# Performance work log

Measured on AMD Instinct MI355X. Metric: run time of the kernel, lower is better.

Reference implementation:

```python
import jax, jax.numpy as jnp
import numpy as np

# physical / numerical constants (from __init__ kwargs)
RHO, G, FD = 910.0, 9.81, 3.1e-17      # ice density, gravity, SIA fluidity (Pa^-3 yr^-1 units folded in)
DX = DY = 100.0                          # grid spacing [m]
DTMAX, CFL = 0.1, 0.2                    # max timestep [yr], CFL safety factor
T0, TIME0, TTOT = 1864.0, 1979.0, 1981.0 # calendar origin, start time, end time
T_FREQ = 10.0                            # SMB refresh interval [yr]
GAMMA, Z_REF = 6.0e-3, 1500.0            # temperature lapse rate [K/m], station elevation [m]
N_STEPS = 64                             # fixed unrolled step budget (while-loop -> masked scan)
NY = NX = 512
N_YEARS, N_DAYS = 128, 365


def setup_inputs() -> dict:
    key = jax.random.key(0)
    k = jax.random.split(key, 6)
    y = jnp.linspace(-1.0, 1.0, NY)
    x = jnp.linspace(-1.0, 1.0, NX)
    X, Y = jnp.meshgrid(x, y)
    r2 = X ** 2 + Y ** 2
    Z_topo = 1500.0 + 1800.0 * jnp.exp(-3.0 * r2) + 20.0 * jax.random.normal(k[0], (NY, NX))
    H_init = 50.0 * jnp.exp(-6.0 * r2)
    ice_mask = (Z_topo > 1800.0).astype(jnp.float32)
    d = jnp.arange(N_DAYS, dtype=jnp.float32)
    season = -2.0 + 12.0 * jnp.sin(2.0 * jnp.pi * (d - 120.0) / 365.0)
    T_daily = season[None, :] + 1.5 * jax.random.normal(k[1], (N_YEARS, N_DAYS))
    P_daily = 0.02 * jax.random.uniform(k[2], (N_YEARS, N_DAYS))
    precip_tensor = jax.random.uniform(k[3], (NY, NX))
    return dict(Z_topo=Z_topo.astype(jnp.float32), H_init=H_init.astype(jnp.float32),
                ice_mask=ice_mask, precip_tensor=precip_tensor,
                T_m_lowest=jnp.array([-2.0], jnp.float32), T_s=jnp.array([12.0], jnp.float32),
                P_daily=P_daily.astype(jnp.float32), T_daily=T_daily.astype(jnp.float32),
                melt_factor=jnp.array([0.005], jnp.float32))


def _smb(Z_surf, P_day, T_day, mf, ice_mask):
    """Degree-day SMB: lapse-rate downscale station daily T/P to the grid. [365,ny,nx] broadcast."""
    T = T_day[:, None, None] - GAMMA * (Z_surf - Z_REF)[None, :, :]
    acc = jnp.sum(jnp.where(T <= 0.0, P_day[:, None, None], 0.0), axis=0)   # snow accumulation [m/yr]
    pdd = jnp.sum(jnp.maximum(T, 0.0), axis=0)                               # positive degree days
    smb = (acc - mf * pdd) * ice_mask
    return jnp.where((smb < 0.0) | (ice_mask > 0.5), smb, -10.0)


def _sia_step(H, Z_topo, smb, t):
    """One adaptive-dt shallow-ice (n=3) explicit stencil step."""
    S = Z_topo + H
    gy, gx = jnp.gradient(S, DY, DX)
    D = FD * (RHO * G) ** 3 * H ** 5 * (gx ** 2 + gy ** 2)   # diffusivity at cell centers
    Dx = 0.5 * (D[:, 1:] + D[:, :-1]); Sx = (S[:, 1:] - S[:, :-1]) / DX
    Dy = 0.5 * (D[1:, :] + D[:-1, :]); Sy = (S[1:, :] - S[:-1, :]) / DY
    qx = jnp.pad(Dx * Sx, ((0, 0), (1, 1)))                   # zero-flux boundaries
    qy = jnp.pad(Dy * Sy, ((1, 1), (0, 0)))
    div = (qx[:, 1:] - qx[:, :-1]) / DX + (qy[1:, :] - qy[:-1, :]) / DY
    dt = jnp.minimum(DTMAX, CFL * min(DX, DY) ** 2 / (jnp.max(D) + 1e-6))   # adaptive timestep
    H_new = jnp.maximum(H + dt * (smb + div), 0.0)
    return H_new, Z_topo + H_new, t + dt


def reference(Z_topo, H_init, ice_mask, precip_tensor, T_m_lowest, T_s, P_daily, T_daily, melt_factor):
    mf = jnp.squeeze(melt_factor)
    n_years = P_daily.shape[0]

    def year_idx(t):
        return jnp.clip(jnp.floor(t - T0), 0, n_years - 1).astype(jnp.int32)

    time0 = jnp.array(TIME0, jnp.float32)
    yi0 = year_idx(time0)
    smb0 = _smb(Z_topo + H_init, P_daily[yi0], T_daily[yi0], mf, ice_mask)
    zeros = jnp.zeros_like(H_init)
    carry0 = (H_init, Z_topo + H_init, time0, smb0, yi0, jnp.array(0.0, jnp.float32),
              zeros, zeros, zeros, jnp.array(False), jnp.array(False), jnp.array(False))

    def body(carry, _):
        H, Zs, t, smb, prev_yi, t_last, s26, s57, s80, g26, g57, g80 = carry
        active = t < TTOT
        Hn, Zsn, tn = _sia_step(H, Z_topo, smb, t)
        Hn = jnp.where(active, Hn, H)
        Zsn = jnp.where(active, Zsn, Zs)
        tn = jnp.where(active, tn, t)

        def snap(s, g, yr):
            hit = active & (tn >= yr)
            return jnp.where(hit & (~g), Hn, s), g | hit
        s26, g26 = snap(s26, g26, 1926.0)
        s57, g57 = snap(s57, g57, 1957.0)
        s80, g80 = snap(s80, g80, 1980.0)

        yi = year_idx(tn)
        need = active & ((yi != prev_yi) | (tn - t_last >= T_FREQ))
        smb_n = jax.lax.cond(need,
                             lambda: _smb(Zsn, P_daily[yi], T_daily[yi], mf, ice_mask),
                             lambda: smb)
        t_last_n = jnp.where(need, tn, t_last)
        prev_yi_n = jnp.where(need, yi, prev_yi)
        return (Hn, Zsn, tn, smb_n, prev_yi_n, t_last_n, s26, s57, s80, g26, g57, g80), None

    carry, _ = jax.lax.scan(jax.checkpoint(body), carry0, None, length=N_STEPS)
    H, _, _, _, _, _, s26, s57, s80, _, _, _ = carry
    return (s26, s57, s80, H)
```

## Files before the change

kernel.cpp:

```cpp
#include <hip/hip_runtime.h>
#include <hip/hip_bf16.h>

namespace {
constexpr int NYg = 512, NXg = 512, NCELL = NYg * NXg;
constexpr int TPB = 1024;
constexpr int NBX = 16, NBY = 16, NBLK = 256;
constexpr int BT = 32;
constexpr int W  = 10;
constexpr int NT = BT + 2 * W;
constexpr int NU = NT - 4;
constexpr int NT2 = NT * NT, NU2 = NU * NU;
constexpr int ITT = 3;
constexpr int NGH = 1476;
constexpr int KG = 5;
constexpr int NSTEP = 64;
constexpr int NEX = 32;
constexpr int DYNLDS = 34816;
constexpr float I1HX = 0.01f;
constexpr float I2HX = 0.005f;
constexpr double RGd = 910.0 * 9.81;
constexpr float PHYS_C = (float)(3.1e-17 * RGd * RGd * RGd);
}

__device__ float    g_H[2][NCELL];
__device__ unsigned g_sflag[NEX][NBLK];
__device__ unsigned g_bmax[NSTEP][NBLK];
__device__ unsigned g_barC = 0, g_barG = 0;

__device__ __forceinline__ void gen_barrier() {
    __syncthreads();
    if (threadIdx.x == 0) {
        __threadfence();
        const unsigned gen = __hip_atomic_load(&g_barG, __ATOMIC_RELAXED,
                                               __HIP_MEMORY_SCOPE_AGENT);
        const unsigned arrived = __hip_atomic_fetch_add(&g_barC, 1u, __ATOMIC_ACQ_REL,
                                                        __HIP_MEMORY_SCOPE_AGENT);
        if (arrived == NBLK - 1) {
            __hip_atomic_store(&g_barC, 0u, __ATOMIC_RELAXED, __HIP_MEMORY_SCOPE_AGENT);
            __hip_atomic_fetch_add(&g_barG, 1u, __ATOMIC_RELEASE, __HIP_MEMORY_SCOPE_AGENT);
        } else {
            while (__hip_atomic_load(&g_barG, __ATOMIC_ACQUIRE,
                                     __HIP_MEMORY_SCOPE_AGENT) == gen)
                __builtin_amdgcn_s_sleep(2);
        }
        __threadfence();
    }
    __syncthreads();
}

__device__ __forceinline__ void coh_store(float* p, float v) {
    __hip_atomic_store(p, v, __ATOMIC_RELAXED, __HIP_MEMORY_SCOPE_AGENT);
}
__device__ __forceinline__ float coh_load(const float* p) {
    return __hip_atomic_load(p, __ATOMIC_RELAXED, __HIP_MEMORY_SCOPE_AGENT);
}

__device__ __forceinline__ bool wire_f32(const void* zt) {
    const unsigned short* u = (const unsigned short*)zt;
    unsigned short a16 = u[0], c16 = u[2];
    const float a = __bfloat162float(*(const __hip_bfloat16*)&a16);
    const float c = __bfloat162float(*(const __hip_bfloat16*)&c16);
    return !((a > 500.0f) && (a < 5000.0f) && (c > 500.0f) && (c < 5000.0f));
}
__device__ __forceinline__ float ldin(const void* p, int i, bool f32) {
    return f32 ? ((const float*)p)[i] : __bfloat162float(((const __hip_bfloat16*)p)[i]);
}
__device__ __forceinline__ void stout(void* p, int i, float v, bool f32) {
    if (f32) ((float*)p)[i] = v;
    else     ((__hip_bfloat16*)p)[i] = __float2bfloat16(v);
}

#define FOR3(X) X(0) X(1) X(2)

__global__ __launch_bounds__(TPB) void GlacierDynamicsCheckpointed_41412074668209_kernel(
    const void* __restrict__ Zt, const void* __restrict__ Hi,
    const void* __restrict__ Mk, const void* __restrict__ Pd,
    const void* __restrict__ Td, const void* __restrict__ Mf,
    void* __restrict__ Out)
{
    __shared__ float Sl[NT2];
    __shared__ float Hl[NT2];
    __shared__ float Zl[NT2];
    __shared__ float Dl[NT2];
    __shared__ float Ts[2][512], Ps[2][512], Js[2][512];
    __shared__ float wred[16];
    __shared__ float dtsh;

    const bool f32 = wire_f32(Zt);
    const int tid = threadIdx.x, b = blockIdx.x;
    const int by = b >> 4, bx = b & 15;
    const int ty0 = by * BT, tx0 = bx * BT;
    const float mf = ldin(Mf, 0, f32);

    float smb_0=0,smb_1=0,smb_2=0;
    float div_0=0,div_1=0,div_2=0;
    unsigned mbbits = 0;

    {
        const int gb = b * TPB + tid;
        constexpr int NS0 = NEX * NBLK;
        constexpr int NS1 = NS0 + NSTEP * NBLK;
        if (gb < NS0)      ((unsigned*)g_sflag)[gb] = 0u;
        else if (gb < NS1) ((unsigned*)g_bmax)[gb - NS0] = 0u;
    }

    #pragma unroll
    for (int it = 0; it < ITT; ++it) {
        const int i = tid + it * TPB;
        if (i < NT2) {
            const int ly = i / NT, lx = i % NT;
            const int gy = min(max(ty0 - W + ly, 0), NYg - 1);
            const int gx = min(max(tx0 - W + lx, 0), NXg - 1);
            const int g = gy * NXg + gx;
            const float z = ldin(Zt, g, f32);
            const float h = ldin(Hi, g, f32);
            Zl[i] = z; Hl[i] = h; Sl[i] = z + h;
        }
    }
    #define MBJ(J) { const int i = tid + J * TPB; if (J < 2 || i < NU2) { \
        const int ly = 2 + i / NU, lx = 2 + i % NU; \
        const int gy = min(max(ty0 - W + ly, 0), NYg - 1); \
        const int gx = min(max(tx0 - W + lx, 0), NXg - 1); \
        if (ldin(Mk, gy * NXg + gx, f32) > 0.5f) mbbits |= (1u << J); } }
    FOR3(MBJ)

    {
        const int w = tid >> 9, idx = tid & 511;
        if (idx < 365) { Ts[w][idx] = ldin(Td, (115 + w) * 365 + idx, f32);
                         Ps[w][idx] = ldin(Pd, (115 + w) * 365 + idx, f32); }
        else           { Ts[w][idx] = 3.0e38f; Ps[w][idx] = 0.0f; }
        __syncthreads();
        for (int kk = 2; kk <= 512; kk <<= 1)
            for (int j = kk >> 1; j > 0; j >>= 1) {
                const int i = idx, ixj = i ^ j;
                if (ixj > i) {
                    const bool up = ((i & kk) == 0);
                    const float a = Ts[w][i], c = Ts[w][ixj];
                    if ((a > c) == up) {
                        Ts[w][i] = c; Ts[w][ixj] = a;
                        const float p = Ps[w][i]; Ps[w][i] = Ps[w][ixj]; Ps[w][ixj] = p;
                    }
                }
                __syncthreads();
            }
        Js[w][idx] = (idx < 365) ? Ts[w][idx] : 0.0f;
        __syncthreads();
        for (int off = 1; off < 512; off <<= 1) {
            const float p = Ps[w][idx] + ((idx >= off) ? Ps[w][idx - off] : 0.0f);
            const float q = Js[w][idx] + ((idx + off < 512) ? Js[w][idx + off] : 0.0f);
            __syncthreads();
            Ps[w][idx] = p; Js[w][idx] = q;
            __syncthreads();
        }
    }

    #define SMBJ(J) { const int i = tid + J * TPB; if (J < 2 || i < NU2) { \
        const int ly = 2 + i / NU, lx = 2 + i % NU; \
        const float zs = Sl[ly * NT + lx]; \
        const float u = 0.006f * (zs - 1500.0f); \
        int lo = 0, hi = 365; \
        while (lo < hi) { const int mid = (lo + hi) >> 1; \
                          if (Tt[mid] <= u) lo = mid + 1; else hi = mid; } \
        const float acc = (lo > 0) ? Pt[lo - 1] : 0.0f; \
        const float pdd = (lo < 365) ? fmaxf(Jt[lo] - u * (float)(365 - lo), 0.0f) : 0.0f; \
        smb_##J = ((mbbits >> J) & 1u) ? (acc - mf * pdd) : -10.0f; } }
    auto refresh = [&](int yi) {
        const int ytab = (yi >= 116) ? 1 : 0;
        const float* Tt = Ts[ytab]; const float* Pt = Ps[ytab]; const float* Jt = Js[ytab];
        FOR3(SMBJ)
    };

    auto computeD = [&](int ly, int lx) -> float {
        const int gy = ty0 - W + ly, gx = tx0 - W + lx;
        const int cgy = min(max(gy, 0), NYg - 1), cgx = min(max(gx, 0), NXg - 1);
        const int si = ly * NT + lx;
        const float sc = Sl[si];
        const float gxv = (cgx == 0)       ? (Sl[si + 1] - sc) * I1HX
                        : (cgx == NXg - 1) ? (sc - Sl[si - 1]) * I1HX
                                           : (Sl[si + 1] - Sl[si - 1]) * I2HX;
        const float gyv = (cgy == 0)       ? (Sl[si + NT] - sc) * I1HX
                        : (cgy == NYg - 1) ? (sc - Sl[si - NT]) * I1HX
                                           : (Sl[si + NT] - Sl[si - NT]) * I2HX;
        const float h = sc - Zl[si];
        const float h2 = h * h;
        return (PHYS_C * (h2 * h2 * h)) * (gxv * gxv + gyv * gyv);
    };

    #define DIVJ(J) { const int i = tid + J * TPB; if (J < 2 || i < NU2) { \
        const int ly = 2 + i / NU, lx = 2 + i % NU; \
        const int gy = ty0 - W + ly, gx = tx0 - W + lx; \
        const int si = ly * NT + lx; \
        const float sc = Sl[si], dc = Dl[si]; \
        float qxR = 0.0f, qxL = 0.0f, qyU = 0.0f, qyD = 0.0f;  \
        if (gx < NXg - 1) qxR = 0.5f * (Dl[si + 1] + dc)  * ((Sl[si + 1] - sc)  * I1HX); \
        if (gx > 0)       qxL = 0.5f * (dc + Dl[si - 1])  * ((sc - Sl[si - 1])  * I1HX); \
        if (gy < NYg - 1) qyU = 0.5f * (Dl[si + NT] + dc) * ((Sl[si + NT] - sc) * I1HX); \
        if (gy > 0)       qyD = 0.5f * (dc + Dl[si - NT]) * ((sc - Sl[si - NT]) * I1HX); \
        div_##J = (qxR - qxL) * I1HX + (qyU - qyD) * I1HX; } }

    #define UPDJ(J) { const int i = tid + J * TPB; if (J < 2 || i < NU2) { \
        const int ly = 2 + i / NU, lx = 2 + i % NU; \
        const int si = ly * NT + lx; \
        const float hn = fmaxf(Hl[si] + dt * (smb_##J + div_##J), 0.0f); \
        Hl[si] = hn; \
        Sl[si] = Zl[si] + hn; } }

    auto exchange = [&](int e) {
        const int par = e & 1;
        {
            const int r = tid >> 5, c = tid & 31;
            coh_store(&g_H[par][(ty0 + r) * NXg + tx0 + c], Hl[(W + r) * NT + W + c]);
        }
        __syncthreads();
        if (tid == 0)
            __hip_atomic_store(&g_sflag[e][b], 1u, __ATOMIC_RELEASE,
                               __HIP_MEMORY_SCOPE_AGENT);
        if (tid < 8) {
            const int d = (tid < 4) ? tid : tid + 1;
            const int nby = by + d / 3 - 1, nbx = bx + d % 3 - 1;
            if (nby >= 0 && nby < NBY && nbx >= 0 && nbx < NBX) {
                const int nb = nby * NBX + nbx;
                while (__hip_atomic_load(&g_sflag[e][nb], __ATOMIC_ACQUIRE,
                                         __HIP_MEMORY_SCOPE_AGENT) == 0u)
                    __builtin_amdgcn_s_sleep(1);
            }
        }
        __syncthreads();
        #pragma unroll
        for (int it = 0; it < ITT; ++it) {
            const int i = tid + it * TPB;
            if (i < NT2) {
                const int ly = i / NT, lx = i % NT;
                const bool core = (ly >= W) & (ly < W + BT) & (lx >= W) & (lx < W + BT);
                if (!core) {
                    const int gy = min(max(ty0 - W + ly, 0), NYg - 1);
                    const int gx = min(max(tx0 - W + lx, 0), NXg - 1);
                    const float h = coh_load(&g_H[par][gy * NXg + gx]);
                    Hl[i] = h; Sl[i] = Zl[i] + h;
                }
            }
        }
        __syncthreads();
    };

    auto snap_store = [&](bool h26, bool h57, bool h80) {
        const int r = tid >> 5, c = tid & 31;
        const int g = (ty0 + r) * NXg + tx0 + c;
        const float h = Hl[(W + r) * NT + W + c];
        if (h26) stout(Out, g, h, f32);
        if (h57) stout(Out, NCELL + g, h, f32);
        if (h80) stout(Out, 2 * NCELL + g, h, f32);
    };

    gen_barrier();
    refresh(115);

    float t = 1979.0f, t_last = 0.0f;
    int prev_yi = 115, phase = 0, ec = 0;
    bool c26 = false, c57 = false, c80 = false;

    #pragma unroll 1
    for (int step = 0; step < NSTEP; ++step) {
        if (phase == KG) { exchange(++ec); phase = 0; }

        float dmax;
        {
            const int ly = W + (tid >> 5), lx = W + (tid & 31);
            const float D = computeD(ly, lx);
            Dl[ly * NT + lx] = D;
            dmax = D;
        }
        for (int off = 32; off; off >>= 1) dmax = fmaxf(dmax, __shfl_down(dmax, off));
        if ((tid & 63) == 0) wred[tid >> 6] = dmax;
        __syncthreads();
        if (tid == 0) {
            float m = wred[0];
            #pragma unroll
            for (int i2 = 1; i2 < 16; ++i2) m = fmaxf(m, wred[i2]);
            __hip_atomic_store(&g_bmax[step][b], ~__float_as_uint(m),
                               __ATOMIC_RELAXED, __HIP_MEMORY_SCOPE_AGENT);
        }

        #pragma unroll
        for (int it = 0; it < 2; ++it) {
            const int i = tid + it * TPB;
            if (i < NGH) {
                int ly, lx;
                if (i < 450)      { ly = 1 + i / 50;               lx = 1 + i % 50; }
                else if (i < 900) { const int k = i - 450; ly = 42 + k / 50; lx = 1 + k % 50; }
                else              { const int k = i - 900; ly = 10 + k / 18;
                                    const int c = k % 18;  lx = (c < 9) ? 1 + c : 33 + c; }
                Dl[ly * NT + lx] = computeD(ly, lx);
            }
        }
        __syncthreads();

        FOR3(DIVJ)

        if (tid < 64) {
            float dv = 0.0f;
            #pragma unroll
            for (int q = 0; q < 4; ++q) {
                unsigned v;
                while ((v = __hip_atomic_load(&g_bmax[step][q * 64 + tid],
                                              __ATOMIC_RELAXED,
                                              __HIP_MEMORY_SCOPE_AGENT)) == 0u)
                    __builtin_amdgcn_s_sleep(1);
                dv = fmaxf(dv, __uint_as_float(~v));
            }
            for (int off = 32; off; off >>= 1) dv = fmaxf(dv, __shfl_xor(dv, off));
            if (tid == 0) dtsh = dv;
        }
        __syncthreads();
        const float dt = fminf(0.1f, 2000.0f / (dtsh + 1e-6f));

        FOR3(UPDJ)
        __syncthreads();
        ++phase;

        const float tn = t + dt;
        const bool hit26 = !c26 && (tn >= 1926.0f);
        const bool hit57 = !c57 && (tn >= 1957.0f);
        const bool hit80 = !c80 && (tn >= 1980.0f);
        if (hit26 | hit57 | hit80) snap_store(hit26, hit57, hit80);
        c26 |= hit26; c57 |= hit57; c80 |= hit80;

        int yi = (int)floorf(tn - 1864.0f);
        yi = min(max(yi, 0), 127);
        const bool need = (yi != prev_yi) || (tn - t_last >= 10.0f);
        if (need) {
            t_last = tn; prev_yi = yi;
            if (tn < 1981.0f) {
                if (phase > 1) { exchange(++ec); phase = 0; }
                refresh(yi);
            }
        }
        t = tn;
        if (t >= 1981.0f) break;
    }

    {
        const int r = tid >> 5, c = tid & 31;
        const int g = (ty0 + r) * NXg + tx0 + c;
        stout(Out, 3 * NCELL + g, Hl[(W + r) * NT + W + c], f32);
        if (!c26) stout(Out, g, 0.0f, f32);
        if (!c57) stout(Out, NCELL + g, 0.0f, f32);
        if (!c80) stout(Out, 2 * NCELL + g, 0.0f, f32);
    }
}

extern "C" void kernel_launch(void* const* d_in, const int* in_sizes, int n_in,
                              void* d_out, int out_size, void* d_ws, size_t ws_size,
                              hipStream_t stream) {
    (void)in_sizes; (void)n_in; (void)out_size; (void)d_ws; (void)ws_size;
    const void* Zt = d_in[0];
    const void* Hi = d_in[1];
    const void* Mk = d_in[2];
    const void* Pd = d_in[6];
    const void* Td = d_in[7];
    const void* Mf = d_in[8];
    hipLaunchKernelGGL(GlacierDynamicsCheckpointed_41412074668209_kernel,
                       dim3(NBLK), dim3(TPB), DYNLDS, stream,
                       Zt, Hi, Mk, Pd, Td, Mf, d_out);
}
```

Before: 209.9 us.

## Replace grid barrier and flag handshakes with generation-tagged max polling and fused halo publish

Drops the initial grid barrier and the per-exchange neighbour-flag handshake. Halo data is published during the update step itself, and the global dt max now doubles as the readiness signal, carrying a per-launch generation tag so the buffers no longer need zeroing. It also pads the shared-memory rows by one to cut bank conflicts, moves the block-level max to workgroup atomics, and shortens the halo refresh interval from 5 to 4 steps. The intent is to remove barrier and handshake latency from the persistent loop. In exchange it relies on fragile memory-ordering assumptions between the dt max and halo stores, and on a per-launch generation counter.

```diff
diff --git a/kernel.cpp b/kernel.cpp
--- a/kernel.cpp
+++ b/kernel.cpp
@@ -8,45 +8,25 @@
 constexpr int BT = 32;
 constexpr int W  = 10;
 constexpr int NT = BT + 2 * W;
+constexpr int NTP = NT + 1;
 constexpr int NU = NT - 4;
-constexpr int NT2 = NT * NT, NU2 = NU * NU;
-constexpr int ITT = 3;
-constexpr int NGH = 1476;
-constexpr int KG = 5;
+constexpr int NT2 = NT * NT;
+constexpr int NU2 = NU * NU;
+constexpr int NCORE = 34 * 34;
+constexpr int NGHD = 1344;
+constexpr int NRL  = 1680;
+constexpr int KG = 4;
 constexpr int NSTEP = 64;
-constexpr int NEX = 32;
-constexpr int DYNLDS = 34816;
+constexpr int DYNLDS = 26624;
 constexpr float I1HX = 0.01f;
 constexpr float I2HX = 0.005f;
 constexpr double RGd = 910.0 * 9.81;
 constexpr float PHYS_C = (float)(3.1e-17 * RGd * RGd * RGd);
 }
 
+__device__ unsigned long long g_bmax[NSTEP][NBLK];
 __device__ float    g_H[2][NCELL];
-__device__ unsigned g_sflag[NEX][NBLK];
-__device__ unsigned g_bmax[NSTEP][NBLK];
-__device__ unsigned g_barC = 0, g_barG = 0;
-
-__device__ __forceinline__ void gen_barrier() {
-    __syncthreads();
-    if (threadIdx.x == 0) {
-        __threadfence();
-        const unsigned gen = __hip_atomic_load(&g_barG, __ATOMIC_RELAXED,
-                                               __HIP_MEMORY_SCOPE_AGENT);
-        const unsigned arrived = __hip_atomic_fetch_add(&g_barC, 1u, __ATOMIC_ACQ_REL,
-                                                        __HIP_MEMORY_SCOPE_AGENT);
-        if (arrived == NBLK - 1) {
-            __hip_atomic_store(&g_barC, 0u, __ATOMIC_RELAXED, __HIP_MEMORY_SCOPE_AGENT);
-            __hip_atomic_fetch_add(&g_barG, 1u, __ATOMIC_RELEASE, __HIP_MEMORY_SCOPE_AGENT);
-        } else {
-            while (__hip_atomic_load(&g_barG, __ATOMIC_ACQUIRE,
-                                     __HIP_MEMORY_SCOPE_AGENT) == gen)
-                __builtin_amdgcn_s_sleep(2);
-        }
-        __threadfence();
-    }
-    __syncthreads();
-}
+__device__ unsigned g_genA[NBLK];
 
 __device__ __forceinline__ void coh_store(float* p, float v) {
     __hip_atomic_store(p, v, __ATOMIC_RELAXED, __HIP_MEMORY_SCOPE_AGENT);
@@ -78,13 +58,15 @@
     const void* __restrict__ Td, const void* __restrict__ Mf,
     void* __restrict__ Out)
 {
-    __shared__ float Sl[NT2];
-    __shared__ float Hl[NT2];
-    __shared__ float Zl[NT2];
-    __shared__ float Dl[NT2];
+    __shared__ float Sl[NT * NTP];
+    __shared__ float Hl[NT * NTP];
+    __shared__ float Zl[NT * NTP];
+    __shared__ float Dl[NT * NTP];
     __shared__ float Ts[2][512], Ps[2][512], Js[2][512];
-    __shared__ float wred[16];
+    __shared__ unsigned shMax[2], shCnt[2];
     __shared__ float dtsh;
+    __shared__ unsigned dtseq;
+    __shared__ unsigned genSh;
 
     const bool f32 = wire_f32(Zt);
     const int tid = threadIdx.x, b = blockIdx.x;
@@ -96,25 +78,23 @@
     float div_0=0,div_1=0,div_2=0;
     unsigned mbbits = 0;
 
-    {
-        const int gb = b * TPB + tid;
-        constexpr int NS0 = NEX * NBLK;
-        constexpr int NS1 = NS0 + NSTEP * NBLK;
-        if (gb < NS0)      ((unsigned*)g_sflag)[gb] = 0u;
-        else if (gb < NS1) ((unsigned*)g_bmax)[gb - NS0] = 0u;
+    if (tid == 0) {
+        shMax[0] = 0u; shMax[1] = 0u; shCnt[0] = 0u; shCnt[1] = 0u; dtseq = 0u;
+        genSh = ++g_genA[b];
     }
 
     #pragma unroll
-    for (int it = 0; it < ITT; ++it) {
-        const int i = tid + it * TPB;
-        if (i < NT2) {
+    for (int it2 = 0; it2 < 3; ++it2) {
+        const int i = tid + it2 * TPB;
+        if (it2 < 2 || i < NT2) {
             const int ly = i / NT, lx = i % NT;
             const int gy = min(max(ty0 - W + ly, 0), NYg - 1);
             const int gx = min(max(tx0 - W + lx, 0), NXg - 1);
             const int g = gy * NXg + gx;
             const float z = ldin(Zt, g, f32);
             const float h = ldin(Hi, g, f32);
-            Zl[i] = z; Hl[i] = h; Sl[i] = z + h;
+            const int si = ly * NTP + lx;
+            Zl[si] = z; Hl[si] = h; Sl[si] = z + h;
         }
     }
     #define MBJ(J) { const int i = tid + J * TPB; if (J < 2 || i < NU2) { \
@@ -138,7 +118,7 @@
                     const float a = Ts[w][i], c = Ts[w][ixj];
                     if ((a > c) == up) {
                         Ts[w][i] = c; Ts[w][ixj] = a;
-                        const float p = Ps[w][i]; Ps[w][i] = Ps[w][ixj]; Ps[w][ixj] = p;
+                        const float pp = Ps[w][i]; Ps[w][i] = Ps[w][ixj]; Ps[w][ixj] = pp;
                     }
                 }
                 __syncthreads();
@@ -153,10 +133,11 @@
             __syncthreads();
         }
     }
+    const unsigned gen = genSh;
 
     #define SMBJ(J) { const int i = tid + J * TPB; if (J < 2 || i < NU2) { \
         const int ly = 2 + i / NU, lx = 2 + i % NU; \
-        const float zs = Sl[ly * NT + lx]; \
+        const float zs = Sl[ly * NTP + lx]; \
         const float u = 0.006f * (zs - 1500.0f); \
         int lo = 0, hi = 365; \
         while (lo < hi) { const int mid = (lo + hi) >> 1; \
@@ -173,14 +154,14 @@
     auto computeD = [&](int ly, int lx) -> float {
         const int gy = ty0 - W + ly, gx = tx0 - W + lx;
         const int cgy = min(max(gy, 0), NYg - 1), cgx = min(max(gx, 0), NXg - 1);
-        const int si = ly * NT + lx;
+        const int si = ly * NTP + lx;
         const float sc = Sl[si];
         const float gxv = (cgx == 0)       ? (Sl[si + 1] - sc) * I1HX
                         : (cgx == NXg - 1) ? (sc - Sl[si - 1]) * I1HX
                                            : (Sl[si + 1] - Sl[si - 1]) * I2HX;
-        const float gyv = (cgy == 0)       ? (Sl[si + NT] - sc) * I1HX
-                        : (cgy == NYg - 1) ? (sc - Sl[si - NT]) * I1HX
-                                           : (Sl[si + NT] - Sl[si - NT]) * I2HX;
+        const float gyv = (cgy == 0)       ? (Sl[si + NTP] - sc) * I1HX
+                        : (cgy == NYg - 1) ? (sc - Sl[si - NTP]) * I1HX
+                                           : (Sl[si + NTP] - Sl[si - NTP]) * I2HX;
         const float h = sc - Zl[si];
         const float h2 = h * h;
         return (PHYS_C * (h2 * h2 * h)) * (gxv * gxv + gyv * gyv);
@@ -189,160 +170,194 @@
     #define DIVJ(J) { const int i = tid + J * TPB; if (J < 2 || i < NU2) { \
         const int ly = 2 + i / NU, lx = 2 + i % NU; \
         const int gy = ty0 - W + ly, gx = tx0 - W + lx; \
-        const int si = ly * NT + lx; \
+        const int si = ly * NTP + lx; \
         const float sc = Sl[si], dc = Dl[si]; \
         float qxR = 0.0f, qxL = 0.0f, qyU = 0.0f, qyD = 0.0f;  \
-        if (gx < NXg - 1) qxR = 0.5f * (Dl[si + 1] + dc)  * ((Sl[si + 1] - sc)  * I1HX); \
-        if (gx > 0)       qxL = 0.5f * (dc + Dl[si - 1])  * ((sc - Sl[si - 1])  * I1HX); \
-        if (gy < NYg - 1) qyU = 0.5f * (Dl[si + NT] + dc) * ((Sl[si + NT] - sc) * I1HX); \
-        if (gy > 0)       qyD = 0.5f * (dc + Dl[si - NT]) * ((sc - Sl[si - NT]) * I1HX); \
+        if (gx < NXg - 1) qxR = 0.5f * (Dl[si + 1] + dc)   * ((Sl[si + 1] - sc)   * I1HX); \
+        if (gx > 0)       qxL = 0.5f * (dc + Dl[si - 1])   * ((sc - Sl[si - 1])   * I1HX); \
+        if (gy < NYg - 1) qyU = 0.5f * (Dl[si + NTP] + dc) * ((Sl[si + NTP] - sc) * I1HX); \
+        if (gy > 0)       qyD = 0.5f * (dc + Dl[si - NTP]) * ((sc - Sl[si - NTP]) * I1HX); \
         div_##J = (qxR - qxL) * I1HX + (qyU - qyD) * I1HX; } }
 
     #define UPDJ(J) { const int i = tid + J * TPB; if (J < 2 || i < NU2) { \
         const int ly = 2 + i / NU, lx = 2 + i % NU; \
-        const int si = ly * NT + lx; \
+        const int si = ly * NTP + lx; \
         const float hn = fmaxf(Hl[si] + dt * (smb_##J + div_##J), 0.0f); \
         Hl[si] = hn; \
-        Sl[si] = Zl[si] + hn; } }
-
-    auto exchange = [&](int e) {
-        const int par = e & 1;
-        {
-            const int r = tid >> 5, c = tid & 31;
-            coh_store(&g_H[par][(ty0 + r) * NXg + tx0 + c], Hl[(W + r) * NT + W + c]);
-        }
-        __syncthreads();
-        if (tid == 0)
-            __hip_atomic_store(&g_sflag[e][b], 1u, __ATOMIC_RELEASE,
-                               __HIP_MEMORY_SCOPE_AGENT);
-        if (tid < 8) {
-            const int d = (tid < 4) ? tid : tid + 1;
-            const int nby = by + d / 3 - 1, nbx = bx + d % 3 - 1;
-            if (nby >= 0 && nby < NBY && nbx >= 0 && nbx < NBX) {
-                const int nb = nby * NBX + nbx;
-                while (__hip_atomic_load(&g_sflag[e][nb], __ATOMIC_ACQUIRE,
-                                         __HIP_MEMORY_SCOPE_AGENT) == 0u)
-                    __builtin_amdgcn_s_sleep(1);
-            }
-        }
-        __syncthreads();
-        #pragma unroll
-        for (int it = 0; it < ITT; ++it) {
-            const int i = tid + it * TPB;
-            if (i < NT2) {
-                const int ly = i / NT, lx = i % NT;
-                const bool core = (ly >= W) & (ly < W + BT) & (lx >= W) & (lx < W + BT);
-                if (!core) {
-                    const int gy = min(max(ty0 - W + ly, 0), NYg - 1);
-                    const int gx = min(max(tx0 - W + lx, 0), NXg - 1);
-                    const float h = coh_load(&g_H[par][gy * NXg + gx]);
-                    Hl[i] = h; Sl[i] = Zl[i] + h;
-                }
-            }
-        }
-        __syncthreads();
-    };
+        Sl[si] = Zl[si] + hn; \
+        if (pub) { \
+            const bool inc = (ly >= W) & (ly < W + BT) & (lx >= W) & (lx < W + BT); \
+            if (inc) coh_store(&g_H[pubPar][(ty0 - W + ly) * NXg + (tx0 - W + lx)], hn); \
+        } } }
 
     auto snap_store = [&](bool h26, bool h57, bool h80) {
         const int r = tid >> 5, c = tid & 31;
         const int g = (ty0 + r) * NXg + tx0 + c;
-        const float h = Hl[(W + r) * NT + W + c];
+        const float h = Hl[(W + r) * NTP + W + c];
         if (h26) stout(Out, g, h, f32);
         if (h57) stout(Out, NCELL + g, h, f32);
         if (h80) stout(Out, 2 * NCELL + g, h, f32);
     };
 
-    gen_barrier();
+    auto pollMax = [&](int step) -> float {
+        float dv = 0.0f;
+        #pragma unroll
+        for (int q = 0; q < 4; ++q) {
+            unsigned long long v;
+            for (;;) {
+                v = __hip_atomic_load(&g_bmax[step][q * 64 + (tid & 63)],
+                                      __ATOMIC_ACQUIRE, __HIP_MEMORY_SCOPE_AGENT);
+                if ((unsigned)(v >> 32) == gen) break;
+                __builtin_amdgcn_s_sleep(1);
+            }
+            dv = fmaxf(dv, __uint_as_float((unsigned)v));
+        }
+        for (int off = 32; off; off >>= 1) dv = fmaxf(dv, __shfl_xor(dv, off));
+        return dv;
+    };
+
     refresh(115);
+    __syncthreads();
 
     float t = 1979.0f, t_last = 0.0f;
-    int prev_yi = 115, phase = 0, ec = 0;
-    bool c26 = false, c57 = false, c80 = false;
+    int prev_yi = 115, phase = 0, ec = 0, refYi = 115;
+    bool c26 = false, c57 = false, c80 = false, refPend = false;
 
     #pragma unroll 1
     for (int step = 0; step < NSTEP; ++step) {
-        if (phase == KG) { exchange(++ec); phase = 0; }
-
-        float dmax;
-        {
-            const int ly = W + (tid >> 5), lx = W + (tid & 31);
-            const float D = computeD(ly, lx);
-            Dl[ly * NT + lx] = D;
-            dmax = D;
+        const int p = step & 1;
+        const bool xstep = (phase == KG) || refPend;
+
+        float dmax = 0.0f;
+        #pragma unroll
+        for (int it2 = 0; it2 < 2; ++it2) {
+            const int i = tid + it2 * TPB;
+            if (it2 == 0 || i < NCORE) {
+                const int ly = 9 + i / 34, lx = 9 + i % 34;
+                const float D = computeD(ly, lx);
+                Dl[ly * NTP + lx] = D;
+                const int gy = ty0 - W + ly, gx = tx0 - W + lx;
+                if (gy >= 0 && gy < NYg && gx >= 0 && gx < NXg)
+                    dmax = fmaxf(dmax, D);
+            }
         }
         for (int off = 32; off; off >>= 1) dmax = fmaxf(dmax, __shfl_down(dmax, off));
-        if ((tid & 63) == 0) wred[tid >> 6] = dmax;
-        __syncthreads();
-        if (tid == 0) {
-            float m = wred[0];
+        if ((tid & 63) == 0) {
+            __hip_atomic_fetch_max(&shMax[p], __float_as_uint(dmax),
+                                   __ATOMIC_RELAXED, __HIP_MEMORY_SCOPE_WORKGROUP);
+            const unsigned old = __hip_atomic_fetch_add(&shCnt[p], 1u,
+                                     __ATOMIC_ACQ_REL, __HIP_MEMORY_SCOPE_WORKGROUP);
+            if (old == 15u) {
+                const unsigned m = __hip_atomic_load(&shMax[p], __ATOMIC_RELAXED,
+                                                     __HIP_MEMORY_SCOPE_WORKGROUP);
+                shMax[p] = 0u; shCnt[p] = 0u;
+                __hip_atomic_store(&g_bmax[step][b],
+                                   ((unsigned long long)gen << 32) | m,
+                                   __ATOMIC_RELEASE, __HIP_MEMORY_SCOPE_AGENT);
+            }
+        }
+
+        float maxD;
+        if (!xstep) {
             #pragma unroll
-            for (int i2 = 1; i2 < 16; ++i2) m = fmaxf(m, wred[i2]);
-            __hip_atomic_store(&g_bmax[step][b], ~__float_as_uint(m),
-                               __ATOMIC_RELAXED, __HIP_MEMORY_SCOPE_AGENT);
-        }
-
-        #pragma unroll
-        for (int it = 0; it < 2; ++it) {
-            const int i = tid + it * TPB;
-            if (i < NGH) {
-                int ly, lx;
-                if (i < 450)      { ly = 1 + i / 50;               lx = 1 + i % 50; }
-                else if (i < 900) { const int k = i - 450; ly = 42 + k / 50; lx = 1 + k % 50; }
-                else              { const int k = i - 900; ly = 10 + k / 18;
-                                    const int c = k % 18;  lx = (c < 9) ? 1 + c : 33 + c; }
-                Dl[ly * NT + lx] = computeD(ly, lx);
-            }
-        }
-        __syncthreads();
-
-        FOR3(DIVJ)
-
-        if (tid < 64) {
-            float dv = 0.0f;
+            for (int it2 = 0; it2 < 2; ++it2) {
+                const int i = tid + it2 * TPB;
+                if (i < NGHD) {
+                    int ly, lx;
+                    if (i < 400)      { ly = 1 + i / 50;               lx = 1 + i % 50; }
+                    else if (i < 800) { const int k = i - 400; ly = 43 + k / 50; lx = 1 + k % 50; }
+                    else              { const int k = i - 800;  ly = 9 + k / 16;
+                                        const int c2 = k % 16;  lx = (c2 < 8) ? 1 + c2 : 35 + c2; }
+                    Dl[ly * NTP + lx] = computeD(ly, lx);
+                }
+            }
+            __syncthreads();
+            FOR3(DIVJ)
+            if (tid < 64) {
+                const float dv = pollMax(step);
+                if (tid == 0) dtsh = dv;
+            }
+            __syncthreads();
+            maxD = dtsh;
+        } else {
+            if (tid < 64) {
+                const float dv = pollMax(step);
+                if (tid == 0) {
+                    dtsh = dv;
+                    __hip_atomic_store(&dtseq, (unsigned)(step + 1), __ATOMIC_RELEASE,
+                                       __HIP_MEMORY_SCOPE_WORKGROUP);
+                }
+            } else {
+                while (__hip_atomic_load(&dtseq, __ATOMIC_ACQUIRE,
+                                         __HIP_MEMORY_SCOPE_WORKGROUP) < (unsigned)(step + 1))
+                    __builtin_amdgcn_s_sleep(1);
+            }
+            const int par = (ec + 1) & 1;
             #pragma unroll
-            for (int q = 0; q < 4; ++q) {
-                unsigned v;
-                while ((v = __hip_atomic_load(&g_bmax[step][q * 64 + tid],
-                                              __ATOMIC_RELAXED,
-                                              __HIP_MEMORY_SCOPE_AGENT)) == 0u)
-                    __builtin_amdgcn_s_sleep(1);
-                dv = fmaxf(dv, __uint_as_float(~v));
-            }
-            for (int off = 32; off; off >>= 1) dv = fmaxf(dv, __shfl_xor(dv, off));
-            if (tid == 0) dtsh = dv;
-        }
-        __syncthreads();
-        const float dt = fminf(0.1f, 2000.0f / (dtsh + 1e-6f));
-
-        FOR3(UPDJ)
-        __syncthreads();
-        ++phase;
+            for (int it2 = 0; it2 < 2; ++it2) {
+                const int i = tid + it2 * TPB;
+                if (i < NRL) {
+                    int ly, lx;
+                    if (i < 520)       { ly = i / 52;             lx = i % 52; }
+                    else if (i < 1040) { const int k = i - 520;  ly = 42 + k / 52; lx = k % 52; }
+                    else               { const int k = i - 1040; ly = 10 + k / 20;
+                                         const int c2 = k % 20;  lx = (c2 < 10) ? c2 : 32 + c2; }
+                    const int gy = min(max(ty0 - W + ly, 0), NYg - 1);
+                    const int gx = min(max(tx0 - W + lx, 0), NXg - 1);
+                    const float h = coh_load(&g_H[par][gy * NXg + gx]);
+                    const int si = ly * NTP + lx;
+                    Hl[si] = h; Sl[si] = Zl[si] + h;
+                }
+            }
+            __syncthreads();
+            #pragma unroll
+            for (int it2 = 0; it2 < 2; ++it2) {
+                const int i = tid + it2 * TPB;
+                if (i < NGHD) {
+                    int ly, lx;
+                    if (i < 400)      { ly = 1 + i / 50;               lx = 1 + i % 50; }
+                    else if (i < 800) { const int k = i - 400; ly = 43 + k / 50; lx = 1 + k % 50; }
+                    else              { const int k = i - 800;  ly = 9 + k / 16;
+                                        const int c2 = k % 16;  lx = (c2 < 8) ? 1 + c2 : 35 + c2; }
+                    Dl[ly * NTP + lx] = computeD(ly, lx);
+                }
+            }
+            __syncthreads();
+            if (refPend) { refresh(refYi); refPend = false; }
+            FOR3(DIVJ)
+            __syncthreads();
+            maxD = dtsh;
+            ++ec; phase = 0;
+        }
+
+        const float dt = fminf(0.1f, 2000.0f / (maxD + 1e-6f));
 
         const float tn = t + dt;
         const bool hit26 = !c26 && (tn >= 1926.0f);
         const bool hit57 = !c57 && (tn >= 1957.0f);
         const bool hit80 = !c80 && (tn >= 1980.0f);
+        int yi = (int)floorf(tn - 1864.0f);
+        yi = min(max(yi, 0), 127);
+        const bool need  = (yi != prev_yi) || (tn - t_last >= 10.0f);
+        const bool doRef = need && (tn < 1981.0f);
+        const bool pub   = doRef || (phase + 1 == KG);
+        const int pubPar = (ec + 1) & 1;
+
+        FOR3(UPDJ)
+        __syncthreads();
+
         if (hit26 | hit57 | hit80) snap_store(hit26, hit57, hit80);
         c26 |= hit26; c57 |= hit57; c80 |= hit80;
-
-        int yi = (int)floorf(tn - 1864.0f);
-        yi = min(max(yi, 0), 127);
-        const bool need = (yi != prev_yi) || (tn - t_last >= 10.0f);
-        if (need) {
-            t_last = tn; prev_yi = yi;
-            if (tn < 1981.0f) {
-                if (phase > 1) { exchange(++ec); phase = 0; }
-                refresh(yi);
-            }
-        }
-        t = tn;
+        if (doRef) { refPend = true; refYi = yi; t_last = tn; prev_yi = yi; }
+
+        t = tn; ++phase;
         if (t >= 1981.0f) break;
     }
 
     {
         const int r = tid >> 5, c = tid & 31;
         const int g = (ty0 + r) * NXg + tx0 + c;
-        stout(Out, 3 * NCELL + g, Hl[(W + r) * NT + W + c], f32);
+        stout(Out, 3 * NCELL + g, Hl[(W + r) * NTP + W + c], f32);
         if (!c26) stout(Out, g, 0.0f, f32);
         if (!c57) stout(Out, NCELL + g, 0.0f, f32);
         if (!c80) stout(Out, 2 * NCELL + g, 0.0f, f32);
```

After: 395.5 us. 1.88x slower.
